# Performance work log

Hardware: AMD Instinct MI355X
Metric: run time of the kernel (lower is better)

## Reference

```python
import jax, jax.numpy as jnp
import numpy as np

# Dimensions
B, T, H = 4, 4096, 2048          # batch, seq, hidden
NH = 16                           # total hash heads = (max_ngram-1)*n_head_per_ngram
PER_HEAD_VOCAB = 100000
DH = 64                           # per-head embedding dim
E = NH * DH                       # engram_hidden_size = 1024
G = 4                             # hc_mult
K = 4                             # kernel_size
DIL = 3                           # dilation = max_ngram_size
EPS_RMS = 1.1920929e-07           # torch RMSNorm default eps (fp32 finfo eps)
EPS_SC = 1e-5                     # ShortConv RMSNorm eps


def setup_inputs() -> dict:
    key = jax.random.key(0)
    ks = jax.random.split(key, 12)
    hidden_states = jax.random.normal(ks[0], (T, B, H), dtype=jnp.float32)
    hash_ids = jax.random.randint(ks[1], (B, T, NH), 0, PER_HEAD_VOCAB)
    emb_table = jax.random.normal(ks[2], (NH * PER_HEAD_VOCAB, DH), dtype=jnp.float32)
    s = 0.02
    key_W = jax.random.normal(ks[3], (G, H, E), dtype=jnp.float32) * s
    key_b = jax.random.normal(ks[4], (G, H), dtype=jnp.float32) * s
    value_W = jax.random.normal(ks[5], (H, E), dtype=jnp.float32) * s
    value_b = jax.random.normal(ks[6], (H,), dtype=jnp.float32) * s
    norm1_w = jnp.ones((G, H), dtype=jnp.float32)
    norm2_w = jnp.ones((G, H), dtype=jnp.float32)
    sc_norm_w = jnp.ones((G, H), dtype=jnp.float32)
    conv_w = jax.random.normal(ks[7], (G * H, K), dtype=jnp.float32) * 0.1
    return {"hidden_states": hidden_states, "hash_ids": hash_ids, "emb_table": emb_table,
            "key_W": key_W, "key_b": key_b, "value_W": value_W, "value_b": value_b,
            "norm1_w": norm1_w, "norm2_w": norm2_w, "sc_norm_w": sc_norm_w, "conv_w": conv_w}


def _rms(x, eps):
    return x * jax.lax.rsqrt(jnp.mean(x * x, axis=-1, keepdims=True) + eps)


def reference(hidden_states, hash_ids, emb_table, key_W, key_b, value_W, value_b,
              norm1_w, norm2_w, sc_norm_w, conv_w):
    # --- precompute_embeddings: hashed multi-head gather ---
    offsets = jnp.arange(NH, dtype=hash_ids.dtype) * PER_HEAD_VOCAB
    emb = emb_table[hash_ids + offsets]              # [B,T,NH,DH]
    emb = emb.reshape(B, T, E)                       # [B,T,E]

    # --- forward ---
    hs = jnp.transpose(hidden_states, (1, 0, 2))     # [B,T,H]
    # per-group key projection + RMSNorm (vectorized over G)
    keys = jnp.einsum('bte,ghe->btgh', emb, key_W) + key_b   # [B,T,G,H]
    nk = _rms(keys, EPS_RMS) * norm1_w               # [B,T,G,H]
    nq = _rms(hs, EPS_RMS)[:, :, None, :] * norm2_w  # [B,T,G,H]
    gate = jnp.sum(nk * nq, axis=-1) / np.sqrt(H)    # [B,T,G]
    gate = jnp.sqrt(jnp.maximum(jnp.abs(gate), 1e-6)) * jnp.sign(gate)
    gate = jax.nn.sigmoid(gate)[..., None]           # [B,T,G,1]
    value = gate * (emb @ value_W.T + value_b)[:, :, None, :]   # [B,T,G,H]

    # --- ShortConv: per-group RMSNorm -> causal dilated depthwise conv -> SiLU ---
    xn = _rms(value, EPS_SC) * sc_norm_w             # [B,T,G,H]
    x_bct = xn.reshape(B, T, G * H).transpose(0, 2, 1)  # [B,G*H,T]
    y = jax.lax.conv_general_dilated(
        x_bct, conv_w[:, None, :],                   # rhs [C,1,K]
        window_strides=(1,), padding=[((K - 1) * DIL, 0)],
        rhs_dilation=(DIL,), dimension_numbers=('NCH', 'OIH', 'NCH'),
        feature_group_count=G * H)                   # [B,G*H,T]
    y = jax.nn.silu(y)
    y = y.transpose(0, 2, 1).reshape(B, T, G, H)

    out = (value + y).mean(axis=2)                   # [B,T,H]
    return jnp.transpose(out, (1, 0, 2))             # [S,B,H]
```

## Files before the change

kernel.cpp:

```cpp
#include <hip/hip_runtime.h>
#include <hip/hip_bf16.h>

#define BB 4
#define TT 4096
#define HH 2048
#define NHH 16
#define VOC 100000
#define EE 1024
#define GG 4
#define BT (BB*TT)
#define NKEY (GG*HH)
#define NTOT (NKEY+HH)
#define NPART 32
#define TCV 48

static constexpr float EPS_RMS = 1.1920929e-07f;
static constexpr float EPS_SC  = 1e-5f;
static constexpr float INV_SQRT_H = 0.02209708691207961f;

using f32x4 = __attribute__((ext_vector_type(4))) float;
using f32x2 = __attribute__((ext_vector_type(2))) float;
using s8v   = __attribute__((ext_vector_type(8))) short;
using gvoid = __attribute__((address_space(1))) const void;
using lvoid = __attribute__((address_space(3))) void;

__device__ __forceinline__ unsigned short f2bf(float f){
  union { __hip_bfloat16 h; unsigned short u; } cv;
  cv.h = __float2bfloat16(f);
  return cv.u;
}
__device__ __forceinline__ float bf2f(unsigned short u){
  union { float f; unsigned u; } cv;
  cv.u = ((unsigned)u) << 16;
  return cv.f;
}
__device__ __forceinline__ s8v pack8(float4 v0, float4 v1){
  s8v o;
  o[0]=(short)f2bf(v0.x); o[1]=(short)f2bf(v0.y); o[2]=(short)f2bf(v0.z); o[3]=(short)f2bf(v0.w);
  o[4]=(short)f2bf(v1.x); o[5]=(short)f2bf(v1.y); o[6]=(short)f2bf(v1.z); o[7]=(short)f2bf(v1.w);
  return o;
}

__global__ __launch_bounds__(256) void convw_pack(const float* __restrict__ kW,
    const float* __restrict__ vW, unsigned short* __restrict__ Bpk){
  const int nb = blockIdx.x;
  const int t = threadIdx.x, lane = t&63, q = t>>6;
  const int n = nb*16 + (lane&15);
  const float* src = (n < NKEY) ? (kW + (size_t)n*EE) : (vW + (size_t)(n-NKEY)*EE);
  #pragma unroll
  for (int i=0;i<8;i++){
    const int kb = q*8 + i;
    const int k0 = kb*32 + (lane>>4)*8;
    float4 v0 = *(const float4*)(src + k0);
    float4 v1 = *(const float4*)(src + k0 + 4);
    *(s8v*)(Bpk + (size_t)(nb*32 + kb)*512 + lane*8) = pack8(v0, v1);
  }
}

__global__ __launch_bounds__(256) void prep_kern(const int* __restrict__ hids,
    const float* __restrict__ table, unsigned short* __restrict__ emb,
    const float* __restrict__ hs, float* __restrict__ rq,
    unsigned short* __restrict__ hsbf){
  const int p = blockIdx.x, tid = threadIdx.x;
  const int e = tid*4, head = e>>6, d = e&63;
  const long row = (long)hids[p*NHH + head] + (long)head*VOC;
  const float4 v = *(const float4*)(table + row*64 + d);
  ushort4 o; o.x=f2bf(v.x); o.y=f2bf(v.y); o.z=f2bf(v.z); o.w=f2bf(v.w);
  *(ushort4*)(emb + (size_t)p*EE + e) = o;
  const int b = p>>12, t = p&4095;
  const float* hrow = hs + ((size_t)t*BB + b)*HH;
  const int e8 = tid*8;
  float4 v0 = *(const float4*)(hrow+e8);
  float4 v1 = *(const float4*)(hrow+e8+4);
  *(s8v*)(hsbf + (size_t)p*HH + e8) = pack8(v0, v1);
  float s = v0.x*v0.x+v0.y*v0.y+v0.z*v0.z+v0.w*v0.w
          + v1.x*v1.x+v1.y*v1.y+v1.z*v1.z+v1.w*v1.w;
  #pragma unroll
  for (int of=32;of>=1;of>>=1) s += __shfl_xor(s,of);
  __shared__ float red[4];
  if ((tid&63)==0) red[tid>>6] = s;
  __syncthreads();
  if (tid==0){
    float tot = red[0]+red[1]+red[2]+red[3];
    rq[p] = rsqrtf(tot*(1.0f/HH) + EPS_RMS);
  }
}

__global__ __launch_bounds__(512, 2) void gemm8(
    const unsigned short* __restrict__ A, const unsigned short* __restrict__ Bpk,
    const float* __restrict__ key_b, const float* __restrict__ value_b,
    const float* __restrict__ n1w, const float* __restrict__ n2w,
    const unsigned short* __restrict__ hsbf, unsigned short* __restrict__ vlinb,
    f32x2* __restrict__ sdp, float* __restrict__ vsqp)
{
  __shared__ unsigned short sh[65536];
  const int tid = threadIdx.x, w = tid>>6, l = tid&63;
  const int wm = w>>2, wn = w&3;
  const int lg = l&15, lr = l>>4;
  const int wg  = blockIdx.x;
  const int swz = (wg&7)*320 + (wg>>3);
  const int tM  = swz/40, tN = swz - tM*40;
  const int Mrow0 = tM*256, Nrow0 = tN*256;

  const int lp = l>>3, lcs = (l&7)^lp;
  const size_t aoffT = (size_t)(Mrow0 + w*16 + lp)*EE + lcs*8;
  const int c0 = lr ^ (lg&7);
  const unsigned aBase = (unsigned)(wm*8192 + lg*64);
  const unsigned bof0 = (unsigned)(tN*16 + wn*4 + 0)*32u*512u + (unsigned)l*8u;
  const unsigned bof1 = (unsigned)(tN*16 + wn*4 + 1)*32u*512u + (unsigned)l*8u;
  const unsigned bof2 = (unsigned)(tN*16 + wn*4 + 2)*32u*512u + (unsigned)l*8u;
  const unsigned bof3 = (unsigned)(tN*16 + wn*4 + 3)*32u*512u + (unsigned)l*8u;

  f32x4 acc[8][4] = {};
  s8v aR0[4], aR1[4], bR0[4], bR1[4];

#define BAR() { asm volatile("" ::: "memory"); __builtin_amdgcn_s_barrier(); asm volatile("" ::: "memory"); }
#define WAITV(N) asm volatile("s_waitcnt vmcnt(" #N ")" ::: "memory")

#define STG_A(J, KT, SB) { \
    const unsigned short* s_ = A + aoffT + (J)*131072 + (KT)*64; \
    const unsigned d_ = (SB)*16384 + (J)*8192 + w*1024; \
    __builtin_amdgcn_global_load_lds((gvoid*)s_,        (lvoid*)(sh + d_),       16, 0, 0); \
    __builtin_amdgcn_global_load_lds((gvoid*)(s_+8192), (lvoid*)(sh + d_ + 512), 16, 0, 0); }
#define STAGE_A(KT, SB) { STG_A(0,KT,SB); STG_A(1,KT,SB); }

#define RD_A(CB, KK, MH, DST) { \
    const unsigned short* p_ = sh + (CB)*16384 + aBase; \
    const unsigned ck_ = (unsigned)((c0 ^ ((KK)<<2))<<3); \
    DST[0] = *(const s8v*)(p_ + ((MH)*4+0)*1024 + ck_); \
    DST[1] = *(const s8v*)(p_ + ((MH)*4+1)*1024 + ck_); \
    DST[2] = *(const s8v*)(p_ + ((MH)*4+2)*1024 + ck_); \
    DST[3] = *(const s8v*)(p_ + ((MH)*4+3)*1024 + ck_); }

#define GLB(KT, KK, DST) { \
    const unsigned short* q_ = Bpk + (unsigned)((KT)*2+(KK))*512u; \
    DST[0] = *(const s8v*)(q_ + bof0); \
    DST[1] = *(const s8v*)(q_ + bof1); \
    DST[2] = *(const s8v*)(q_ + bof2); \
    DST[3] = *(const s8v*)(q_ + bof3); }

#define MM(MH, AF, BF) { \
    __builtin_amdgcn_s_setprio(1); \
    _Pragma("unroll") \
    for (int mf=0; mf<4; mf++) \
      _Pragma("unroll") \
      for (int nf=0; nf<4; nf++) \
        acc[(MH)*4+mf][nf] = __builtin_amdgcn_mfma_f32_16x16x32_bf16(AF[mf], BF[nf], acc[(MH)*4+mf][nf], 0,0,0); \
    __builtin_amdgcn_s_setprio(0); }

#define TILE(CB, NB, KT0, KT1, DOST) { \
    BAR(); \
    if (DOST) STAGE_A(KT1, NB); \
    GLB(KT0, 1, bR1); \
    RD_A(CB,1,0,aR1); \
    MM(0, aR0, bR0); \
    RD_A(CB,0,1,aR0); \
    MM(0, aR1, bR1); \
    RD_A(CB,1,1,aR1); \
    MM(1, aR0, bR0); \
    WAITV(0); \
    BAR(); \
    GLB(KT1, 0, bR0); \
    RD_A(NB,0,0,aR0); \
    MM(1, aR1, bR1); }

#define TILE_LAST(CB, KT0) { \
    BAR(); \
    GLB(KT0, 1, bR1); \
    RD_A(CB,1,0,aR1); \
    MM(0, aR0, bR0); \
    RD_A(CB,0,1,aR0); \
    MM(0, aR1, bR1); \
    RD_A(CB,1,1,aR1); \
    MM(1, aR0, bR0); \
    MM(1, aR1, bR1); }

  STAGE_A(0, 0);
  STAGE_A(1, 1);
  GLB(0, 0, bR0);
  WAITV(0);
  BAR();
  RD_A(0,0,0,aR0);

  #pragma unroll 1
  for (int i=0; i<7; i++){
    TILE(0, 1, 2*i,   2*i+1, true);
    TILE(1, 0, 2*i+1, 2*i+2, true);
  }
  TILE(0, 1, 14, 15, true);
  TILE_LAST(1, 15);

#undef STG_A
#undef STAGE_A
#undef RD_A
#undef GLB
#undef MM
#undef TILE
#undef TILE_LAST
#undef BAR
#undef WAITV

  __syncthreads();

  const bool isK = (Nrow0 < NKEY);
  float bias[4], cw[4];
  #pragma unroll
  for (int nf=0; nf<4; nf++){
    const int n = Nrow0 + wn*64 + nf*16 + lg;
    if (isK){ bias[nf] = key_b[n]; cw[nf] = n1w[n]*n2w[n]; }
    else    { bias[nf] = value_b[n-NKEY]; cw[nf] = 0.f; }
  }

  if (isK){
    const int g = tN >> 3;
    const int slot = (tN&7)*4 + wn;
    const int colbase = (tN&7)*256;
    unsigned short* hsT = sh;
    char* wreg = ((char*)sh) + 65536 + w*8192;
    #pragma unroll
    for (int half=0; half<2; half++){
      #pragma unroll
      for (int pass=0; pass<8; pass++){
        const int r2 = pass*16 + (tid>>5);
        const int c8 = (tid&31)*8;
        const int p = Mrow0 + half*128 + r2;
        s8v wv = *(const s8v*)(hsbf + (size_t)p*HH + colbase + c8);
        *(s8v*)(hsT + r2*256 + (c8 ^ (((r2>>2)&3)<<4))) = wv;
      }
      __syncthreads();
      if (wm == half){
        #pragma unroll
        for (int pass2=0; pass2<2; pass2++){
          #pragma unroll
          for (int mfs=0; mfs<4; mfs++){
            const int mfa = pass2*4 + mfs;
            #pragma unroll
            for (int rr=0; rr<4; rr++){
              const int rowq = mfs*16 + lr*4 + rr;
              const int rowlh = pass2*64 + rowq;
              float ssq=0.f, dt=0.f;
              #pragma unroll
              for (int nf=0; nf<4; nf++){
                const float c = acc[mfa][nf][rr] + bias[nf];
                const float hv = bf2f(hsT[rowlh*256 + wn*64 + ((nf^lr)<<4) + lg]);
                ssq += c*c;
                dt  += c * cw[nf] * hv;
              }
              f32x2 pr; pr[0]=ssq; pr[1]=dt;
              *(f32x2*)(wreg + rowq*128 + (((lg>>1) ^ (rowq&7))<<4) + ((lg&1)<<3)) = pr;
            }
          }
          {
            const int r = l;
            float ssq=0.f, dt=0.f;
            #pragma unroll
            for (int c=0; c<8; c++){
              f32x4 v = *(const f32x4*)(wreg + r*128 + ((c ^ (r&7))<<4));
              ssq += v[0] + v[2]; dt += v[1] + v[3];
            }
            const int p = Mrow0 + wm*128 + pass2*64 + r;
            f32x2 o2; o2[0]=ssq; o2[1]=dt;
            sdp[(size_t)(p*GG+g)*NPART + slot] = o2;
          }
        }
      }
      __syncthreads();
    }
  } else {
    const int slot = (tN-32)*4 + wn;
    const int h0 = Nrow0 - NKEY + wn*64;
    const int pbase = Mrow0 + wm*128;
    #pragma unroll
    for (int mfa=0; mfa<8; mfa++){
      #pragma unroll
      for (int rr=0; rr<4; rr++){
        const int p = pbase + mfa*16 + lr*4 + rr;
        float ssq=0.f;
        #pragma unroll
        for (int nf=0; nf<4; nf++){
          const float c = acc[mfa][nf][rr] + bias[nf];
          vlinb[(size_t)p*HH + h0 + nf*16 + lg] = f2bf(c);
          ssq += c*c;
        }
        #pragma unroll
        for (int o=1;o<16;o<<=1){ ssq += __shfl_xor(ssq,o); }
        if (lg==0) vsqp[(size_t)p*NPART + slot] = ssq;
      }
    }
  }
}

__global__ __launch_bounds__(256) void scal_kern(const f32x2* __restrict__ sdp,
    const float* __restrict__ vsqp,
    const float* __restrict__ rq, float* __restrict__ gate, float* __restrict__ av){
  const int i = blockIdx.x*256 + threadIdx.x;
  const int p = i>>2;
  float ss=0.f, dd=0.f, vv=0.f;
  const f32x2* sp = sdp + (size_t)i*NPART;
  #pragma unroll
  for (int j=0;j<NPART;j++){ f32x2 v = sp[j]; ss += v[0]; dd += v[1]; }
  #pragma unroll
  for (int j=0;j<NPART;j++){ vv += vsqp[(size_t)p*NPART+j]; }
  const float rk = rsqrtf(ss*(1.0f/HH) + EPS_RMS);
  const float gv = rk * rq[p] * dd * INV_SQRT_H;
  const float sgn = (gv>0.f)?1.f:((gv<0.f)?-1.f:0.f);
  const float g1 = sqrtf(fmaxf(fabsf(gv),1e-6f))*sgn;
  const float gt = 1.f/(1.f+__expf(-g1));
  const float msvl = vv*(1.0f/HH);
  const float a = gt * rsqrtf(gt*gt*msvl + EPS_SC);
  gate[i]=gt; av[i]=a;
}

__device__ __forceinline__ ushort4 ldrow(const unsigned short* __restrict__ v, int b, int t, int h0){
  if (t < 0){ ushort4 z; z.x=0;z.y=0;z.z=0;z.w=0; return z; }
  return *(const ushort4*)(v + (size_t)((b<<12)|t)*HH + h0);
}
__device__ __forceinline__ void ldav(const float* __restrict__ av, int b, int t, float* a){
  if (t < 0){ a[0]=0.f;a[1]=0.f;a[2]=0.f;a[3]=0.f; }
  else { const float4 x = *(const float4*)(av + (size_t)((b<<12)|t)*GG);
         a[0]=x.x;a[1]=x.y;a[2]=x.z;a[3]=x.w; }
}

__global__ __launch_bounds__(256) void conv2_kern(const unsigned short* __restrict__ vlinb,
    const float* __restrict__ gate, const float* __restrict__ av,
    const float* __restrict__ conv_w, const float* __restrict__ scw,
    float* __restrict__ out){
  const int bx = blockIdx.x;
  const int b  = blockIdx.y;
  const int t0 = (bx>>1)*TCV;
  const int h0 = (bx&1)*1024 + threadIdx.x*4;

  float cwv[4][4][4];
  float sc4[4][4];
  #pragma unroll
  for (int g=0; g<4; g++){
    #pragma unroll
    for (int j2=0; j2<4; j2++){
      const int c = g*HH + h0 + j2;
      const float4 wv = *(const float4*)(conv_w + (size_t)c*4);
      cwv[g][j2][0]=wv.x; cwv[g][j2][1]=wv.y; cwv[g][j2][2]=wv.z; cwv[g][j2][3]=wv.w;
      sc4[g][j2] = scw[c];
    }
  }

  #pragma unroll 1
  for (int r=0; r<3; r++){
    const int tf = t0 + r;
    ushort4 w0 = ldrow(vlinb, b, tf-9, h0);
    ushort4 w1 = ldrow(vlinb, b, tf-6, h0);
    ushort4 w2 = ldrow(vlinb, b, tf-3, h0);
    ushort4 w3; w3.x=0;w3.y=0;w3.z=0;w3.w=0;
    float a0[4],a1[4],a2[4],a3[4];
    ldav(av, b, tf-9, a0); ldav(av, b, tf-6, a1); ldav(av, b, tf-3, a2);
    #pragma unroll
    for (int j=0; j<16; j++){
      const int t = tf + 3*j;
      if (t < TT){
        const int p = (b<<12)|t;
        w3 = *(const ushort4*)(vlinb + (size_t)p*HH + h0);
        ldav(av, b, t, a3);
        float gt4[4];
        { const float4 xx = *(const float4*)(gate + (size_t)p*GG);
          gt4[0]=xx.x; gt4[1]=xx.y; gt4[2]=xx.z; gt4[3]=xx.w; }
        float v0[4],v1[4],v2[4],v3[4];
        v0[0]=bf2f(w0.x); v0[1]=bf2f(w0.y); v0[2]=bf2f(w0.z); v0[3]=bf2f(w0.w);
        v1[0]=bf2f(w1.x); v1[1]=bf2f(w1.y); v1[2]=bf2f(w1.z); v1[3]=bf2f(w1.w);
        v2[0]=bf2f(w2.x); v2[1]=bf2f(w2.y); v2[2]=bf2f(w2.z); v2[3]=bf2f(w2.w);
        v3[0]=bf2f(w3.x); v3[1]=bf2f(w3.y); v3[2]=bf2f(w3.z); v3[3]=bf2f(w3.w);
        float4 ov;
        float res[4];
        #pragma unroll
        for (int j2=0; j2<4; j2++){
          float acc = 0.f;
          #pragma unroll
          for (int g=0; g<4; g++){
            float y = cwv[g][j2][0]*a0[g]*v0[j2]
                    + cwv[g][j2][1]*a1[g]*v1[j2]
                    + cwv[g][j2][2]*a2[g]*v2[j2]
                    + cwv[g][j2][3]*a3[g]*v3[j2];
            y *= sc4[g][j2];
            const float sy = y * (1.f/(1.f+__expf(-y)));
            acc += gt4[g]*v3[j2] + sy;
          }
          res[j2] = acc*0.25f;
        }
        ov.x=res[0]; ov.y=res[1]; ov.z=res[2]; ov.w=res[3];
        *(float4*)(out + ((size_t)t*BB + b)*HH + h0) = ov;
      }
      w0=w1; w1=w2; w2=w3;
      #pragma unroll
      for (int g=0; g<4; g++){ a0[g]=a1[g]; a1[g]=a2[g]; a2[g]=a3[g]; }
    }
  }
}

extern "C" void kernel_launch(void* const* d_in, const int* in_sizes, int n_in,
                              void* d_out, int out_size, void* d_ws, size_t ws_size,
                              hipStream_t stream){
  (void)in_sizes; (void)n_in; (void)out_size; (void)ws_size;
  const float* hs    = (const float*)d_in[0];
  const int*   hids  = (const int*)d_in[1];
  const float* table = (const float*)d_in[2];
  const float* keyW  = (const float*)d_in[3];
  const float* keyB  = (const float*)d_in[4];
  const float* valW  = (const float*)d_in[5];
  const float* valB  = (const float*)d_in[6];
  const float* n1w   = (const float*)d_in[7];
  const float* n2w   = (const float*)d_in[8];
  const float* scw   = (const float*)d_in[9];
  const float* convw = (const float*)d_in[10];
  float* out = (float*)d_out;

  char* ws = (char*)d_ws;
  size_t off = 0;
  unsigned short* emb   = (unsigned short*)(ws+off); off += (size_t)BT*EE*2;
  unsigned short* Bpk   = (unsigned short*)(ws+off); off += (size_t)NTOT*EE*2;
  unsigned short* vlinb = (unsigned short*)(ws+off); off += (size_t)BT*HH*2;
  unsigned short* hsbf  = (unsigned short*)(ws+off); off += (size_t)BT*HH*2;
  f32x2* sdp    = (f32x2*)(ws+off); off += (size_t)BT*GG*NPART*8;
  float* vsqp   = (float*)(ws+off); off += (size_t)BT*NPART*4;
  float* rq     = (float*)(ws+off); off += (size_t)BT*4;
  float* gate   = (float*)(ws+off); off += (size_t)BT*GG*4;
  float* av     = (float*)(ws+off); off += (size_t)BT*GG*4;

  convw_pack<<<NTOT/16, 256, 0, stream>>>(keyW, valW, Bpk);
  prep_kern<<<BT, 256, 0, stream>>>(hids, table, emb, hs, rq, hsbf);
  gemm8<<<2560, 512, 0, stream>>>(emb, Bpk, keyB, valB, n1w, n2w, hsbf, vlinb, sdp, vsqp);
  scal_kern<<<(BT*GG)/256, 256, 0, stream>>>(sdp, vsqp, rq, gate, av);
  dim3 cg(((TT + TCV - 1)/TCV)*2, BB);
  conv2_kern<<<cg, 256, 0, stream>>>(vlinb, gate, av, convw, scw, out);
}
```

Before: 616.0 us.

## Restructure GEMM to 4-wave blocks staging both A and B in LDS

The main GEMM moves from 8 waves, each computing a 128x64 subtile with B fragments loaded straight from a pre-packed global layout, to 4 waves, each computing a 128x128 subtile. Both A and B tiles are now staged into a 128KB double-buffered LDS region via global_load_lds. The weight conversion becomes a plain row-major bf16 cast, and the per-row partial-sum slot count drops from 32 to 16 to match the wider wave tiles. The aim is to cut global B traffic and raise MFMA work per LDS read, at the cost of heavy register use (64 accumulators), one block per CU, and a simpler pipeline with less overlap between loads and math.

```diff
diff --git a/kernel.cpp b/kernel.cpp
--- a/kernel.cpp
+++ b/kernel.cpp
@@ -11,7 +11,7 @@
 #define BT (BB*TT)
 #define NKEY (GG*HH)
 #define NTOT (NKEY+HH)
-#define NPART 32
+#define NPART 16
 #define TCV 48
 
 static constexpr float EPS_RMS = 1.1920929e-07f;
@@ -41,20 +41,16 @@
   return o;
 }
 
-__global__ __launch_bounds__(256) void convw_pack(const float* __restrict__ kW,
-    const float* __restrict__ vW, unsigned short* __restrict__ Bpk){
-  const int nb = blockIdx.x;
-  const int t = threadIdx.x, lane = t&63, q = t>>6;
-  const int n = nb*16 + (lane&15);
-  const float* src = (n < NKEY) ? (kW + (size_t)n*EE) : (vW + (size_t)(n-NKEY)*EE);
-  #pragma unroll
-  for (int i=0;i<8;i++){
-    const int kb = q*8 + i;
-    const int k0 = kb*32 + (lane>>4)*8;
-    float4 v0 = *(const float4*)(src + k0);
-    float4 v1 = *(const float4*)(src + k0 + 4);
-    *(s8v*)(Bpk + (size_t)(nb*32 + kb)*512 + lane*8) = pack8(v0, v1);
-  }
+__global__ __launch_bounds__(256) void convw_kern(const float* __restrict__ kW,
+    const float* __restrict__ vW, unsigned short* __restrict__ Wc){
+  const long idx  = (long)blockIdx.x*256 + threadIdx.x;
+  const long base = idx*4;
+  const long KN   = (long)NKEY*EE;
+  float4 v;
+  if (base < KN) v = *(const float4*)(kW + base);
+  else           v = *(const float4*)(vW + (base - KN));
+  ushort4 o; o.x=f2bf(v.x); o.y=f2bf(v.y); o.z=f2bf(v.z); o.w=f2bf(v.w);
+  *(ushort4*)(Wc + base) = o;
 }
 
 __global__ __launch_bounds__(256) void prep_kern(const int* __restrict__ hids,
@@ -86,16 +82,16 @@
   }
 }
 
-__global__ __launch_bounds__(512, 2) void gemm8(
-    const unsigned short* __restrict__ A, const unsigned short* __restrict__ Bpk,
+__global__ __launch_bounds__(256, 1) void gemm4(
+    const unsigned short* __restrict__ A, const unsigned short* __restrict__ Bw,
     const float* __restrict__ key_b, const float* __restrict__ value_b,
     const float* __restrict__ n1w, const float* __restrict__ n2w,
     const unsigned short* __restrict__ hsbf, unsigned short* __restrict__ vlinb,
     f32x2* __restrict__ sdp, float* __restrict__ vsqp)
 {
-  __shared__ unsigned short sh[65536];
+  __shared__ char sh[131072];
   const int tid = threadIdx.x, w = tid>>6, l = tid&63;
-  const int wm = w>>2, wn = w&3;
+  const int wr = w>>1, wc = w&1;
   const int lg = l&15, lr = l>>4;
   const int wg  = blockIdx.x;
   const int swz = (wg&7)*320 + (wg>>3);
@@ -103,146 +99,115 @@
   const int Mrow0 = tM*256, Nrow0 = tN*256;
 
   const int lp = l>>3, lcs = (l&7)^lp;
-  const size_t aoffT = (size_t)(Mrow0 + w*16 + lp)*EE + lcs*8;
+  const size_t aoffS = (size_t)(Mrow0 + w*64 + lp)*EE + lcs*8;
+  const size_t boffS = (size_t)(Nrow0 + w*64 + lp)*EE + lcs*8;
   const int c0 = lr ^ (lg&7);
-  const unsigned aBase = (unsigned)(wm*8192 + lg*64);
-  const unsigned bof0 = (unsigned)(tN*16 + wn*4 + 0)*32u*512u + (unsigned)l*8u;
-  const unsigned bof1 = (unsigned)(tN*16 + wn*4 + 1)*32u*512u + (unsigned)l*8u;
-  const unsigned bof2 = (unsigned)(tN*16 + wn*4 + 2)*32u*512u + (unsigned)l*8u;
-  const unsigned bof3 = (unsigned)(tN*16 + wn*4 + 3)*32u*512u + (unsigned)l*8u;
-
-  f32x4 acc[8][4] = {};
-  s8v aR0[4], aR1[4], bR0[4], bR1[4];
+  const unsigned ck0 = (unsigned)(c0<<4);
+  const unsigned ck1 = (unsigned)((c0^4)<<4);
+  const unsigned aB0 = (unsigned)(wr*16384 + lg*128);
+  const unsigned bB0 = 32768u + (unsigned)(wc*16384 + lg*128);
+
+  f32x4 acc[8][8] = {};
+  s8v a0[8], b0[8], a1[8], b1[8];
 
 #define BAR() { asm volatile("" ::: "memory"); __builtin_amdgcn_s_barrier(); asm volatile("" ::: "memory"); }
-#define WAITV(N) asm volatile("s_waitcnt vmcnt(" #N ")" ::: "memory")
-
-#define STG_A(J, KT, SB) { \
-    const unsigned short* s_ = A + aoffT + (J)*131072 + (KT)*64; \
-    const unsigned d_ = (SB)*16384 + (J)*8192 + w*1024; \
-    __builtin_amdgcn_global_load_lds((gvoid*)s_,        (lvoid*)(sh + d_),       16, 0, 0); \
-    __builtin_amdgcn_global_load_lds((gvoid*)(s_+8192), (lvoid*)(sh + d_ + 512), 16, 0, 0); }
-#define STAGE_A(KT, SB) { STG_A(0,KT,SB); STG_A(1,KT,SB); }
-
-#define RD_A(CB, KK, MH, DST) { \
-    const unsigned short* p_ = sh + (CB)*16384 + aBase; \
-    const unsigned ck_ = (unsigned)((c0 ^ ((KK)<<2))<<3); \
-    DST[0] = *(const s8v*)(p_ + ((MH)*4+0)*1024 + ck_); \
-    DST[1] = *(const s8v*)(p_ + ((MH)*4+1)*1024 + ck_); \
-    DST[2] = *(const s8v*)(p_ + ((MH)*4+2)*1024 + ck_); \
-    DST[3] = *(const s8v*)(p_ + ((MH)*4+3)*1024 + ck_); }
-
-#define GLB(KT, KK, DST) { \
-    const unsigned short* q_ = Bpk + (unsigned)((KT)*2+(KK))*512u; \
-    DST[0] = *(const s8v*)(q_ + bof0); \
-    DST[1] = *(const s8v*)(q_ + bof1); \
-    DST[2] = *(const s8v*)(q_ + bof2); \
-    DST[3] = *(const s8v*)(q_ + bof3); }
-
-#define MM(MH, AF, BF) { \
+#define VM0 asm volatile("s_waitcnt vmcnt(0)" ::: "memory")
+
+#define STAGE16(KT, SB) { \
+    _Pragma("unroll") \
+    for (int j=0;j<8;j++){ \
+      const unsigned short* sa_ = A + aoffS + (size_t)j*8*EE + (KT)*64; \
+      const unsigned short* sb_ = Bw + boffS + (size_t)j*8*EE + (KT)*64; \
+      const unsigned da_ = (SB)*65536 + w*8192 + j*1024; \
+      __builtin_amdgcn_global_load_lds((gvoid*)sa_, (lvoid*)(sh + da_),         16, 0, 0); \
+      __builtin_amdgcn_global_load_lds((gvoid*)sb_, (lvoid*)(sh + da_ + 32768), 16, 0, 0); \
+    } }
+
+#define RD8(CB, BASE, CK, DST) { \
+    _Pragma("unroll") \
+    for (int f=0; f<8; f++) \
+      DST[f] = *(const s8v*)(sh + (CB)*65536 + (BASE) + f*2048 + (CK)); }
+
+#define MM64(AS, BS) { \
     __builtin_amdgcn_s_setprio(1); \
     _Pragma("unroll") \
-    for (int mf=0; mf<4; mf++) \
+    for (int mf=0; mf<8; mf++) \
       _Pragma("unroll") \
-      for (int nf=0; nf<4; nf++) \
-        acc[(MH)*4+mf][nf] = __builtin_amdgcn_mfma_f32_16x16x32_bf16(AF[mf], BF[nf], acc[(MH)*4+mf][nf], 0,0,0); \
+      for (int nf=0; nf<8; nf++) \
+        acc[mf][nf] = __builtin_amdgcn_mfma_f32_16x16x32_bf16(AS[mf], BS[nf], acc[mf][nf], 0,0,0); \
     __builtin_amdgcn_s_setprio(0); }
 
-#define TILE(CB, NB, KT0, KT1, DOST) { \
+#define TILE(CB, NB, KT1, DOST) { \
     BAR(); \
-    if (DOST) STAGE_A(KT1, NB); \
-    GLB(KT0, 1, bR1); \
-    RD_A(CB,1,0,aR1); \
-    MM(0, aR0, bR0); \
-    RD_A(CB,0,1,aR0); \
-    MM(0, aR1, bR1); \
-    RD_A(CB,1,1,aR1); \
-    MM(1, aR0, bR0); \
-    WAITV(0); \
-    BAR(); \
-    GLB(KT1, 0, bR0); \
-    RD_A(NB,0,0,aR0); \
-    MM(1, aR1, bR1); }
-
-#define TILE_LAST(CB, KT0) { \
-    BAR(); \
-    GLB(KT0, 1, bR1); \
-    RD_A(CB,1,0,aR1); \
-    MM(0, aR0, bR0); \
-    RD_A(CB,0,1,aR0); \
-    MM(0, aR1, bR1); \
-    RD_A(CB,1,1,aR1); \
-    MM(1, aR0, bR0); \
-    MM(1, aR1, bR1); }
-
-  STAGE_A(0, 0);
-  STAGE_A(1, 1);
-  GLB(0, 0, bR0);
-  WAITV(0);
-  BAR();
-  RD_A(0,0,0,aR0);
+    if (DOST) STAGE16(KT1, NB); \
+    RD8(CB, aB0, ck0, a0); RD8(CB, bB0, ck0, b0); \
+    RD8(CB, aB0, ck1, a1); RD8(CB, bB0, ck1, b1); \
+    MM64(a0, b0); \
+    MM64(a1, b1); \
+    VM0; \
+    BAR(); }
+
+  STAGE16(0, 0);
+  VM0;
 
   #pragma unroll 1
   for (int i=0; i<7; i++){
-    TILE(0, 1, 2*i,   2*i+1, true);
-    TILE(1, 0, 2*i+1, 2*i+2, true);
-  }
-  TILE(0, 1, 14, 15, true);
-  TILE_LAST(1, 15);
-
-#undef STG_A
-#undef STAGE_A
-#undef RD_A
-#undef GLB
-#undef MM
+    TILE(0, 1, 2*i+1, 1);
+    TILE(1, 0, 2*i+2, 1);
+  }
+  TILE(0, 1, 15, 1);
+  TILE(1, 0, 0, 0);
+
+#undef STAGE16
+#undef RD8
+#undef MM64
 #undef TILE
-#undef TILE_LAST
-#undef BAR
-#undef WAITV
-
-  __syncthreads();
+#undef VM0
+
+  BAR();
 
   const bool isK = (Nrow0 < NKEY);
-  float bias[4], cw[4];
-  #pragma unroll
-  for (int nf=0; nf<4; nf++){
-    const int n = Nrow0 + wn*64 + nf*16 + lg;
+  float bias[8], cw[8];
+  #pragma unroll
+  for (int nf=0; nf<8; nf++){
+    const int n = Nrow0 + wc*128 + nf*16 + lg;
     if (isK){ bias[nf] = key_b[n]; cw[nf] = n1w[n]*n2w[n]; }
     else    { bias[nf] = value_b[n-NKEY]; cw[nf] = 0.f; }
   }
 
   if (isK){
     const int g = tN >> 3;
-    const int slot = (tN&7)*4 + wn;
+    const int slot = (tN&7)*2 + wc;
     const int colbase = (tN&7)*256;
-    unsigned short* hsT = sh;
-    char* wreg = ((char*)sh) + 65536 + w*8192;
+    unsigned short* hsT = (unsigned short*)sh;
+    char* wreg = sh + 65536 + w*8192;
     #pragma unroll
     for (int half=0; half<2; half++){
       #pragma unroll
-      for (int pass=0; pass<8; pass++){
-        const int r2 = pass*16 + (tid>>5);
+      for (int pass=0; pass<16; pass++){
+        const int r2 = pass*8 + (tid>>5);
         const int c8 = (tid&31)*8;
         const int p = Mrow0 + half*128 + r2;
         s8v wv = *(const s8v*)(hsbf + (size_t)p*HH + colbase + c8);
         *(s8v*)(hsT + r2*256 + (c8 ^ (((r2>>2)&3)<<4))) = wv;
       }
       __syncthreads();
-      if (wm == half){
+      if (wr == half){
         #pragma unroll
-        for (int pass2=0; pass2<2; pass2++){
+        for (int p2=0; p2<2; p2++){
           #pragma unroll
           for (int mfs=0; mfs<4; mfs++){
-            const int mfa = pass2*4 + mfs;
+            const int mf = p2*4 + mfs;
             #pragma unroll
             for (int rr=0; rr<4; rr++){
               const int rowq = mfs*16 + lr*4 + rr;
-              const int rowlh = pass2*64 + rowq;
+              const int rowh = p2*64 + rowq;
               float ssq=0.f, dt=0.f;
               #pragma unroll
-              for (int nf=0; nf<4; nf++){
-                const float c = acc[mfa][nf][rr] + bias[nf];
-                const float hv = bf2f(hsT[rowlh*256 + wn*64 + ((nf^lr)<<4) + lg]);
+              for (int nf=0; nf<8; nf++){
+                const float c = acc[mf][nf][rr] + bias[nf];
+                const int col = wc*128 + nf*16 + lg;
+                const float hv = bf2f(hsT[rowh*256 + (col ^ (lr<<4))]);
                 ssq += c*c;
                 dt  += c * cw[nf] * hv;
               }
@@ -258,7 +223,7 @@
               f32x4 v = *(const f32x4*)(wreg + r*128 + ((c ^ (r&7))<<4));
               ssq += v[0] + v[2]; dt += v[1] + v[3];
             }
-            const int p = Mrow0 + wm*128 + pass2*64 + r;
+            const int p = Mrow0 + half*128 + p2*64 + r;
             f32x2 o2; o2[0]=ssq; o2[1]=dt;
             sdp[(size_t)(p*GG+g)*NPART + slot] = o2;
           }
@@ -267,18 +232,18 @@
       __syncthreads();
     }
   } else {
-    const int slot = (tN-32)*4 + wn;
-    const int h0 = Nrow0 - NKEY + wn*64;
-    const int pbase = Mrow0 + wm*128;
+    const int slot = (tN-32)*2 + wc;
+    const int h0 = Nrow0 - NKEY + wc*128;
+    const int pbase = Mrow0 + wr*128;
     #pragma unroll
-    for (int mfa=0; mfa<8; mfa++){
+    for (int mf=0; mf<8; mf++){
       #pragma unroll
       for (int rr=0; rr<4; rr++){
-        const int p = pbase + mfa*16 + lr*4 + rr;
+        const int p = pbase + mf*16 + lr*4 + rr;
         float ssq=0.f;
         #pragma unroll
-        for (int nf=0; nf<4; nf++){
-          const float c = acc[mfa][nf][rr] + bias[nf];
+        for (int nf=0; nf<8; nf++){
+          const float c = acc[mf][nf][rr] + bias[nf];
           vlinb[(size_t)p*HH + h0 + nf*16 + lg] = f2bf(c);
           ssq += c*c;
         }
@@ -414,7 +379,7 @@
   char* ws = (char*)d_ws;
   size_t off = 0;
   unsigned short* emb   = (unsigned short*)(ws+off); off += (size_t)BT*EE*2;
-  unsigned short* Bpk   = (unsigned short*)(ws+off); off += (size_t)NTOT*EE*2;
+  unsigned short* Wc    = (unsigned short*)(ws+off); off += (size_t)NTOT*EE*2;
   unsigned short* vlinb = (unsigned short*)(ws+off); off += (size_t)BT*HH*2;
   unsigned short* hsbf  = (unsigned short*)(ws+off); off += (size_t)BT*HH*2;
   f32x2* sdp    = (f32x2*)(ws+off); off += (size_t)BT*GG*NPART*8;
@@ -423,9 +388,9 @@
   float* gate   = (float*)(ws+off); off += (size_t)BT*GG*4;
   float* av     = (float*)(ws+off); off += (size_t)BT*GG*4;
 
-  convw_pack<<<NTOT/16, 256, 0, stream>>>(keyW, valW, Bpk);
+  convw_kern<<<(NTOT*EE/4)/256, 256, 0, stream>>>(keyW, valW, Wc);
   prep_kern<<<BT, 256, 0, stream>>>(hids, table, emb, hs, rq, hsbf);
-  gemm8<<<2560, 512, 0, stream>>>(emb, Bpk, keyB, valB, n1w, n2w, hsbf, vlinb, sdp, vsqp);
+  gemm4<<<2560, 256, 0, stream>>>(emb, Wc, keyB, valB, n1w, n2w, hsbf, vlinb, sdp, vsqp);
   scal_kern<<<(BT*GG)/256, 256, 0, stream>>>(sdp, vsqp, rq, gate, av);
   dim3 cg(((TT + TCV - 1)/TCV)*2, BB);
   conv2_kern<<<cg, 256, 0, stream>>>(vlinb, gate, av, convw, scw, out);
```

After: 782.4 us. 1.27x slower.
